# Performance work log

Hardware: AMD Instinct MI355X
Metric: run time of the kernel (lower is better)

## Reference

```python
import jax, jax.numpy as jnp
import numpy as np

N_HEAD = 16
HEAD_SIZE = 64
N_EMBD = 1024
B, T = 4, 2048
THETA = 10000.0


def _rope_cos_sin(t_len, dim):
    # freqs: (dim//2,), angles: (T, dim//2)
    inv = 1.0 / (THETA ** (jnp.arange(0, dim, 2, dtype=jnp.float32) / dim))
    ang = jnp.arange(t_len, dtype=jnp.float32)[:, None] * inv[None, :]
    return jnp.cos(ang), jnp.sin(ang)


def _apply_rope(x, cos, sin):
    # x: (B, H, T, hs) -> complex-pair rotation over last dim
    xr = x.reshape(*x.shape[:-1], -1, 2)
    x0, x1 = xr[..., 0], xr[..., 1]
    c = cos[None, None, :, :]
    s = sin[None, None, :, :]
    o0 = x0 * c - x1 * s
    o1 = x0 * s + x1 * c
    return jnp.stack([o0, o1], axis=-1).reshape(x.shape)


def setup_inputs() -> dict:
    key = jax.random.key(0)
    ks = jax.random.split(key, 5)
    scale = 1.0 / np.sqrt(N_EMBD)
    return {
        "x": jax.random.normal(ks[0], (B, T, N_EMBD), dtype=jnp.float32),
        "Wq": jax.random.normal(ks[1], (N_EMBD, N_HEAD * HEAD_SIZE), dtype=jnp.float32) * scale,
        "Wk": jax.random.normal(ks[2], (N_EMBD, N_HEAD * HEAD_SIZE), dtype=jnp.float32) * scale,
        "Wv": jax.random.normal(ks[3], (N_EMBD, N_HEAD * HEAD_SIZE), dtype=jnp.float32) * scale,
        "Wp": jax.random.normal(ks[4], (N_HEAD * HEAD_SIZE, N_EMBD), dtype=jnp.float32) * scale,
        "bp": jnp.zeros((N_EMBD,), dtype=jnp.float32),
    }


def reference(x, Wq, Wk, Wv, Wp, bp):
    Bx, Tx, C = x.shape
    q = (x @ Wq).reshape(Bx, Tx, N_HEAD, HEAD_SIZE).transpose(0, 2, 1, 3)
    k = (x @ Wk).reshape(Bx, Tx, N_HEAD, HEAD_SIZE).transpose(0, 2, 1, 3)
    v = (x @ Wv).reshape(Bx, Tx, N_HEAD, HEAD_SIZE).transpose(0, 2, 1, 3)
    cos, sin = _rope_cos_sin(Tx, HEAD_SIZE)
    q = _apply_rope(q, cos, sin)
    k = _apply_rope(k, cos, sin)
    wei = jnp.einsum('bhqd,bhkd->bhqk', q, k) * (HEAD_SIZE ** -0.5)
    causal = jnp.tril(jnp.ones((Tx, Tx), dtype=bool))
    wei = jnp.where(causal[None, None, :, :], wei, -jnp.inf)
    wei = jax.nn.softmax(wei, axis=-1)
    out = jnp.einsum('bhqk,bhkd->bhqd', wei, v)
    out = out.transpose(0, 2, 1, 3).reshape(Bx, Tx, N_HEAD * HEAD_SIZE)
    return out @ Wp + bp
```

## Files before the change

### kernel.cpp

```cpp
#include <hip/hip_runtime.h>
#include <hip/hip_bf16.h>

#define NH 16
#define HS 64
#define CE 1024
#define BB 4
#define TT 2048

typedef __bf16 bf16;
typedef __bf16 v8bf __attribute__((ext_vector_type(8)));
typedef __bf16 v4bf __attribute__((ext_vector_type(4)));
typedef __bf16 v2bf __attribute__((ext_vector_type(2)));
typedef float v4f __attribute__((ext_vector_type(4)));
typedef float v16f __attribute__((ext_vector_type(16)));

#define GLD16(gp, lp)                                                              \
    __builtin_amdgcn_global_load_lds((const __attribute__((address_space(1))) void*)(gp), \
                                     (__attribute__((address_space(3))) void*)(lp), 16, 0, 0)

#define FENCE() __builtin_amdgcn_sched_barrier(0)
#define BARRIER() { FENCE(); __builtin_amdgcn_s_barrier(); FENCE(); }
#define VM4()  { asm volatile("s_waitcnt vmcnt(4)" ::: "memory"); FENCE(); }
#define VM8()  { asm volatile("s_waitcnt vmcnt(8)" ::: "memory"); FENCE(); }
#define VM0()  { asm volatile("s_waitcnt vmcnt(0)" ::: "memory"); FENCE(); }

__global__ __launch_bounds__(256) void prep_kernel(const float* __restrict__ x,
                                                   const float* __restrict__ W0,
                                                   const float* __restrict__ W1,
                                                   const float* __restrict__ W2,
                                                   const float* __restrict__ W3,
                                                   bf16* __restrict__ xb,
                                                   float2* __restrict__ csQ,
                                                   float2* __restrict__ csK,
                                                   bf16* __restrict__ dqkv,
                                                   bf16* __restrict__ dp) {
    __shared__ bf16 tile[64][66];
    const int bid = blockIdx.x;
    const int tid = threadIdx.x;
    if (bid < 4096) {
        int idx = (bid * 256 + tid) * 8;
        const float4* xp = (const float4*)(x + idx);
        float4 a = xp[0], b = xp[1];
        v8bf o;
        o[0] = (bf16)a.x; o[1] = (bf16)a.y; o[2] = (bf16)a.z; o[3] = (bf16)a.w;
        o[4] = (bf16)b.x; o[5] = (bf16)b.y; o[6] = (bf16)b.z; o[7] = (bf16)b.w;
        *(v8bf*)(xb + idx) = o;
    } else if (bid < 4352) {
        int idx = (bid - 4096) * 256 + tid;
        int t = idx >> 5, i = idx & 31;
        float inv = exp2f(-0.41524101186092034f * (float)i);
        float ang = (float)t * inv;
        float s, c;
        sincosf(ang, &s, &c);
        const float QS = 0.18033688011112042f;
        csK[idx] = make_float2(c, s);
        csQ[idx] = make_float2(c * QS, s * QS);
    } else {
        int idx = bid - 4352;
        int z = idx >> 8, rem = idx & 255;
        const float* W = (z == 0) ? W0 : (z == 1) ? W1 : (z == 2) ? W2 : W3;
        bf16* Wt = (z < 3) ? (dqkv + (size_t)z * 1024 * CE) : dp;
        int k0 = (rem & 15) * 64;
        int n0 = (rem >> 4) * 64;
        int tx = tid & 63;
        int ty = tid >> 6;
        for (int s = 0; s < 16; s++) {
            int r = s * 4 + ty;
            tile[r][tx] = (bf16)W[(size_t)(k0 + r) * CE + n0 + tx];
        }
        __syncthreads();
        for (int s = 0; s < 16; s++) {
            int r = s * 4 + ty;
            Wt[(size_t)(n0 + r) * CE + k0 + tx] = tile[tx][r];
        }
    }
}

#define GSTAGE(AD, BD, kk) {                                                        \
    _Pragma("unroll") for (int p = 0; p < 4; p++)                                   \
        GLD16(Ag + (kk) + (size_t)(p * 32) * CE, (AD) + p * 2048);                  \
    _Pragma("unroll") for (int p = 0; p < 4; p++)                                   \
        GLD16(Bg + (kk) + (size_t)(p * 32) * CE, (BD) + p * 2048); }

#define GCOMPUTE(ASrc, BSrc)                                                        \
    _Pragma("unroll")                                                               \
    for (int kh = 0; kh < 2; kh++) {                                                \
        v8bf af[4], bfr[4];                                                         \
        for (int i = 0; i < 4; i++) {                                               \
            int row = wr * 64 + i * 16 + lane15;                                    \
            af[i] = *(const v8bf*)(&ASrc[row * 64 + (((kh * 4 + quad) ^ (lane15 & 7)) * 8)]); \
        }                                                                           \
        for (int j = 0; j < 4; j++) {                                               \
            int row = wc * 64 + j * 16 + lane15;                                    \
            bfr[j] = *(const v8bf*)(&BSrc[row * 64 + (((kh * 4 + quad) ^ (lane15 & 7)) * 8)]); \
        }                                                                           \
        for (int i = 0; i < 4; i++)                                                 \
            for (int j = 0; j < 4; j++)                                             \
                acc[i][j] = __builtin_amdgcn_mfma_f32_16x16x32_bf16(af[i], bfr[j], acc[i][j], 0, 0, 0); \
    }

#define GEMM_PROLOG(Abuf, Bbuf)                                                     \
    __shared__ __align__(16) bf16 As0[128 * 64];                                    \
    __shared__ __align__(16) bf16 Bs0[128 * 64];                                    \
    __shared__ __align__(16) bf16 As1[128 * 64];                                    \
    __shared__ __align__(16) bf16 Bs1[128 * 64];                                    \
    const int tid = threadIdx.x;                                                    \
    const int lane = tid & 63, wave = tid >> 6;                                     \
    const int lane15 = lane & 15, quad = lane >> 4;                                 \
    const int wr = wave >> 1, wc = wave & 1;                                        \
    const int m0 = blockIdx.y * 128;                                                \
    const int n0 = blockIdx.x * 128;                                                \
    v4f acc[4][4] = {};                                                             \
    const int cm = tid >> 3;                                                        \
    const int ck = ((tid & 7) ^ (cm & 7)) * 8;                                      \
    const bf16* Ag = (Abuf) + (size_t)(m0 + cm) * CE + ck;                          \
    const bf16* Bg = (Bbuf) + (size_t)(n0 + cm) * CE + ck;                          \
    bf16* aD0 = &As0[wave * 512];                                                   \
    bf16* bD0 = &Bs0[wave * 512];                                                   \
    bf16* aD1 = &As1[wave * 512];                                                   \
    bf16* bD1 = &Bs1[wave * 512];

#define GEMM_KLOOP()                                                                \
    GSTAGE(aD0, bD0, 0);                                                            \
    for (int k0 = 0; k0 < CE; k0 += 128) {                                          \
        GSTAGE(aD1, bD1, k0 + 64);                                                  \
        VM8(); BARRIER();                                                           \
        GCOMPUTE(As0, Bs0);                                                         \
        BARRIER();                                                                  \
        GSTAGE(aD0, bD0, (k0 + 128) & 1023);                                        \
        VM8(); BARRIER();                                                           \
        GCOMPUTE(As1, Bs1);                                                         \
        BARRIER();                                                                  \
    }                                                                               \
    VM0();

__global__ __launch_bounds__(256) void gemm_qkv(const bf16* __restrict__ A,
                                                const bf16* __restrict__ Bt,
                                                bf16* __restrict__ Qb_, bf16* __restrict__ Kb_,
                                                bf16* __restrict__ Vt_,
                                                const float2* __restrict__ csQ,
                                                const float2* __restrict__ csK) {
    GEMM_PROLOG(A, Bt)
    GEMM_KLOOP()

    for (int i = 0; i < 4; i++) {
        for (int j = 0; j < 4; j++) {
            int gmb = m0 + wr * 64 + i * 16 + quad * 4;
            int gn = n0 + wc * 64 + j * 16 + lane15;
            int w = gn >> 10;
            int n = gn & 1023;
            int hh = n >> 6, d = n & 63;
            if (w < 2) {
                bf16* out = w ? Kb_ : Qb_;
                const float2* csRow = (w ? csK : csQ) + (d >> 1);
                const int par = gn & 1;
                const int dbase = d & ~1;
                const int b = gmb >> 11, tbase = gmb & 2047;
                const float xv0 = acc[i][j][0], xv1 = acc[i][j][1];
                const float xv2 = acc[i][j][2], xv3 = acc[i][j][3];
                const float pv0 = __shfl_xor(xv0, 1), pv1 = __shfl_xor(xv1, 1);
                const float pv2 = __shfl_xor(xv2, 1), pv3 = __shfl_xor(xv3, 1);
                const float xa = par ? xv2 : xv0, pa = par ? pv2 : pv0;
                const float xb2 = par ? xv3 : xv1, pb = par ? pv3 : pv1;
                const float ua = par ? pa : xa, va = par ? xa : pa;
                const float ub = par ? pb : xb2, vb = par ? xb2 : pb;
                const int ta = tbase + (par << 1), tb = ta + 1;
                const float2 csa = csRow[ta * 32];
                const float2 csb = csRow[tb * 32];
                v2bf sa, sb;
                sa[0] = (bf16)(ua * csa.x - va * csa.y);
                sa[1] = (bf16)(ua * csa.y + va * csa.x);
                sb[0] = (bf16)(ub * csb.x - vb * csb.y);
                sb[1] = (bf16)(ub * csb.y + vb * csb.x);
                bf16* rowp = out + ((size_t)(b * NH + hh)) * TT * HS + dbase;
                *(v2bf*)(rowp + (size_t)ta * HS) = sa;
                *(v2bf*)(rowp + (size_t)tb * HS) = sb;
            } else {
                int b = gmb >> 11, t = gmb & 2047;
                v4bf pack;
                for (int r = 0; r < 4; r++) pack[r] = (bf16)acc[i][j][r];
                *(v4bf*)(&Vt_[(((size_t)(b * NH + hh)) * HS + d) * TT + t]) = pack;
            }
        }
    }
}

__global__ __launch_bounds__(256) void gemm_proj(const bf16* __restrict__ A,
                                                 const bf16* __restrict__ Bt,
                                                 float* __restrict__ Pout,
                                                 const float* __restrict__ bias) {
    GEMM_PROLOG(A, Bt)

    float bb[4];
#pragma unroll
    for (int j = 0; j < 4; j++) bb[j] = bias[n0 + wc * 64 + j * 16 + lane15];

    GEMM_KLOOP()

    for (int i = 0; i < 4; i++) {
        for (int j = 0; j < 4; j++) {
            int gmb = m0 + wr * 64 + i * 16 + quad * 4;
            int gn = n0 + wc * 64 + j * 16 + lane15;
            for (int r = 0; r < 4; r++)
                Pout[(size_t)(gmb + r) * CE + gn] = acc[i][j][r] + bb[j];
        }
    }
}

#define ASTAGE(KD, VD, kv) {                                        \
    GLD16(kg + (size_t)(kv) * HS, (KD));                            \
    GLD16(kg + (size_t)((kv) + 32) * HS, (KD) + 2048);              \
    GLD16(vg + (kv), (VD));                                         \
    GLD16(vg + (kv) + 32 * TT, (VD) + 2048); }

#define ACOMPUTE(KS, VS, KVB)                                                       \
    _Pragma("unroll")                                                               \
    for (int sub = 0; sub < 2; sub++) {                                             \
        const int kvs = (KVB) + sub * 32;                                           \
        if (kvs > q0) break;                                                        \
        const bool diag = (kvs == q0);                                              \
        v16f s = {};                                                                \
        __builtin_amdgcn_s_setprio(1);                                              \
        for (int m = 0; m < 4; m++) {                                               \
            v8bf afr = *(const v8bf*)(&KS[(sub * 32 + lane31) * 64 +                \
                                          (((m << 1) | h) ^ (lane31 & 7)) * 8]);    \
            s = __builtin_amdgcn_mfma_f32_32x32x16_bf16(afr, qf[m], s, 0, 0, 0);    \
        }                                                                           \
        __builtin_amdgcn_s_setprio(0);                                              \
        float p[16];                                                                \
        if (diag) {                                                                 \
            for (int r = 0; r < 16; r++) {                                          \
                int kvr = (r & 3) + 8 * (r >> 2) + 4 * h;                           \
                p[r] = exp2f((kvr <= lane31) ? s[r] : -3.0e38f);                    \
            }                                                                       \
        } else {                                                                    \
            for (int r = 0; r < 16; r++) p[r] = exp2f(s[r]);                        \
        }                                                                           \
        float a8[8];                                                                \
        for (int r = 0; r < 8; r++) a8[r] = p[r] + p[r + 8];                        \
        l_i += ((a8[0] + a8[1]) + (a8[2] + a8[3])) + ((a8[4] + a8[5]) + (a8[6] + a8[7])); \
        union { v4bf v; unsigned long long u; } ch[4];                              \
        for (int g = 0; g < 4; g++)                                                 \
            for (int rr = 0; rr < 4; rr++)                                          \
                ch[g].v[rr] = (bf16)p[g * 4 + rr];                                  \
        __builtin_amdgcn_s_setprio(1);                                              \
        for (int t2 = 0; t2 < 2; t2++) {                                            \
            unsigned long long mine0 = ch[2 * t2].u, mine1 = ch[2 * t2 + 1].u;      \
            unsigned long long send = h ? mine0 : mine1;                            \
            unsigned long long recv = __shfl_xor(send, 32);                         \
            union { v8bf v; unsigned long long u[2]; } bfr2;                        \
            bfr2.u[0] = h ? recv : mine0;                                           \
            bfr2.u[1] = h ? mine1 : recv;                                           \
            int cidx = (((sub << 2) + (t2 << 1) + h) ^ (lane31 & 7)) * 8;           \
            v8bf va0 = *(const v8bf*)(&VS[lane31 * 64 + cidx]);                     \
            o0 = __builtin_amdgcn_mfma_f32_32x32x16_bf16(va0, bfr2.v, o0, 0, 0, 0); \
            v8bf va1 = *(const v8bf*)(&VS[(32 + lane31) * 64 + cidx]);              \
            o1 = __builtin_amdgcn_mfma_f32_32x32x16_bf16(va1, bfr2.v, o1, 0, 0, 0); \
        }                                                                           \
        __builtin_amdgcn_s_setprio(0);                                              \
    }

__global__ __launch_bounds__(256, 4) void attn_kernel(const bf16* __restrict__ Qb,
                                                      const bf16* __restrict__ Kb,
                                                      const bf16* __restrict__ Vt,
                                                      bf16* __restrict__ Ob) {
    __shared__ __align__(16) bf16 Ks0[64 * 64];
    __shared__ __align__(16) bf16 Vs0[64 * 64];
    __shared__ __align__(16) bf16 Ks1[64 * 64];
    __shared__ __align__(16) bf16 Vs1[64 * 64];
    const int tid = threadIdx.x, lane = tid & 63, wave = tid >> 6;
    const int lane31 = lane & 31, h = lane >> 5;
    const int bh = blockIdx.x & 63;
    const int qb = 15 - (int)(blockIdx.x >> 6);
    const int q0 = qb * 128 + wave * 32;
    const bf16* Qp = Qb + (size_t)bh * TT * HS;
    const bf16* Kp = Kb + (size_t)bh * TT * HS;
    const bf16* Vp = Vt + (size_t)bh * HS * TT;

    v8bf qf[4];
    for (int m = 0; m < 4; m++)
        qf[m] = *(const v8bf*)(Qp + (size_t)(q0 + lane31) * HS + m * 16 + h * 8);

    v16f o0 = {}, o1 = {};
    float l_i = 0.f;

    const int kr = tid >> 3, kc = tid & 7;
    const bf16* kg = Kp + kr * HS + ((kc ^ (kr & 7)) * 8);
    const bf16* vg = Vp + (size_t)kr * TT + ((kc ^ (kr & 7)) * 8);
    bf16* ksD0 = &Ks0[wave * 512];
    bf16* vsD0 = &Vs0[wave * 512];
    bf16* ksD1 = &Ks1[wave * 512];
    bf16* vsD1 = &Vs1[wave * 512];

    const int kv_max = qb * 128 + 96;
    ASTAGE(ksD0, vsD0, 0);
    for (int kv0 = 0; kv0 <= kv_max; kv0 += 128) {
        ASTAGE(ksD1, vsD1, kv0 + 64);
        VM4(); BARRIER();
        ACOMPUTE(Ks0, Vs0, kv0);
        BARRIER();
        ASTAGE(ksD0, vsD0, (kv0 + 128) & 2047);
        VM4(); BARRIER();
        ACOMPUTE(Ks1, Vs1, kv0 + 64);
        BARRIER();
    }
    VM0();

    const int b = bh >> 4, hh = bh & 15;
    const int q = q0 + lane31;
    float lt = l_i + __shfl_xor(l_i, 32);
    float invl = 1.f / lt;
    bf16* outRow = Ob + ((size_t)(b * TT + q)) * CE + hh * HS;
    for (int g = 0; g < 4; g++) {
        v4bf w0, w1;
        for (int rr = 0; rr < 4; rr++) {
            w0[rr] = (bf16)(o0[g * 4 + rr] * invl);
            w1[rr] = (bf16)(o1[g * 4 + rr] * invl);
        }
        *(v4bf*)(outRow + g * 8 + h * 4) = w0;
        *(v4bf*)(outRow + 32 + g * 8 + h * 4) = w1;
    }
}

extern "C" void kernel_launch(void* const* d_in, const int* in_sizes, int n_in,
                              void* d_out, int out_size, void* d_ws, size_t ws_size,
                              hipStream_t stream) {
    const float* x  = (const float*)d_in[0];
    const float* Wq = (const float*)d_in[1];
    const float* Wk = (const float*)d_in[2];
    const float* Wv = (const float*)d_in[3];
    const float* Wp = (const float*)d_in[4];
    const float* bp = (const float*)d_in[5];
    char* ws = (char*)d_ws;
    const size_t MB = 1024 * 1024;
    bf16* Xb    = (bf16*)(ws);
    bf16* WqkvT = (bf16*)(ws + 16 * MB);
    bf16* WpT   = (bf16*)(ws + 22 * MB);
    bf16* Qb    = (bf16*)(ws + 24 * MB);
    bf16* Kb    = (bf16*)(ws + 40 * MB);
    bf16* Vt    = (bf16*)(ws + 56 * MB);
    bf16* Ob    = (bf16*)(ws + 72 * MB);
    float2* csQ = (float2*)(ws + 72 * MB);
    float2* csK = (float2*)(ws + 72 * MB + 512 * 1024);

    prep_kernel<<<dim3(5376), dim3(256), 0, stream>>>(x, Wq, Wk, Wv, Wp, Xb, csQ, csK,
                                                      WqkvT, WpT);

    gemm_qkv<<<dim3(24, 64), dim3(256), 0, stream>>>(Xb, WqkvT, Qb, Kb, Vt, csQ, csK);

    attn_kernel<<<dim3(1024), dim3(256), 0, stream>>>(Qb, Kb, Vt, Ob);

    gemm_proj<<<dim3(8, 64), dim3(256), 0, stream>>>(Ob, WpT, (float*)d_out, bp);
}
```

Measured before the change: 261.6 us.

## Double attention block to 8 waves and swizzle GEMM tile order

Each attention block now has 512 threads (8 waves) covering 256 queries, so every staged K/V tile in LDS is reused by twice as many waves and each thread issues half as many global-to-LDS loads. The attention grid interleaves heavy and light causal query blocks to balance work across the device. Separately, the GEMM tiles are remapped in chunks of eight with a serpentine column order to improve L2 locality. The trade-off is a larger block with more registers and barriers, and the longest diagonal blocks get longer.

```diff
diff --git a/kernel.cpp b/kernel.cpp
--- a/kernel.cpp
+++ b/kernel.cpp
@@ -20,7 +20,7 @@
 
 #define FENCE() __builtin_amdgcn_sched_barrier(0)
 #define BARRIER() { FENCE(); __builtin_amdgcn_s_barrier(); FENCE(); }
-#define VM4()  { asm volatile("s_waitcnt vmcnt(4)" ::: "memory"); FENCE(); }
+#define VM2()  { asm volatile("s_waitcnt vmcnt(2)" ::: "memory"); FENCE(); }
 #define VM8()  { asm volatile("s_waitcnt vmcnt(8)" ::: "memory"); FENCE(); }
 #define VM0()  { asm volatile("s_waitcnt vmcnt(0)" ::: "memory"); FENCE(); }
 
@@ -108,8 +108,14 @@
     const int lane = tid & 63, wave = tid >> 6;                                     \
     const int lane15 = lane & 15, quad = lane >> 4;                                 \
     const int wr = wave >> 1, wc = wave & 1;                                        \
-    const int m0 = blockIdx.y * 128;                                                \
-    const int n0 = blockIdx.x * 128;                                                \
+    const int fid = blockIdx.y * gridDim.x + blockIdx.x;                            \
+    const int bchunk = (gridDim.x * gridDim.y) >> 3;                                \
+    const int swzb = (fid & 7) * bchunk + (fid >> 3);                               \
+    const int bmy = swzb / gridDim.x;                                               \
+    const int bnx0 = swzb % gridDim.x;                                              \
+    const int bnx = (bmy & 1) ? (gridDim.x - 1 - bnx0) : bnx0;                      \
+    const int m0 = bmy * 128;                                                       \
+    const int n0 = bnx * 128;                                                       \
     v4f acc[4][4] = {};                                                             \
     const int cm = tid >> 3;                                                        \
     const int ck = ((tid & 7) ^ (cm & 7)) * 8;                                      \
@@ -209,9 +215,7 @@
 
 #define ASTAGE(KD, VD, kv) {                                        \
     GLD16(kg + (size_t)(kv) * HS, (KD));                            \
-    GLD16(kg + (size_t)((kv) + 32) * HS, (KD) + 2048);              \
-    GLD16(vg + (kv), (VD));                                         \
-    GLD16(vg + (kv) + 32 * TT, (VD) + 2048); }
+    GLD16(vg + (kv), (VD)); }
 
 #define ACOMPUTE(KS, VS, KVB)                                                       \
     _Pragma("unroll")                                                               \
@@ -260,7 +264,7 @@
         __builtin_amdgcn_s_setprio(0);                                              \
     }
 
-__global__ __launch_bounds__(256, 4) void attn_kernel(const bf16* __restrict__ Qb,
+__global__ __launch_bounds__(512, 4) void attn_kernel(const bf16* __restrict__ Qb,
                                                       const bf16* __restrict__ Kb,
                                                       const bf16* __restrict__ Vt,
                                                       bf16* __restrict__ Ob) {
@@ -270,9 +274,12 @@
     __shared__ __align__(16) bf16 Vs1[64 * 64];
     const int tid = threadIdx.x, lane = tid & 63, wave = tid >> 6;
     const int lane31 = lane & 31, h = lane >> 5;
-    const int bh = blockIdx.x & 63;
-    const int qb = 15 - (int)(blockIdx.x >> 6);
-    const int q0 = qb * 128 + wave * 32;
+    const int bid = blockIdx.x;
+    const int x8 = bid & 7, jj = bid >> 3;
+    const int bh = x8 + 8 * (jj >> 3);
+    const int s9 = jj & 7;
+    const int qb = (s9 & 1) ? (s9 >> 1) : (7 - (s9 >> 1));
+    const int q0 = qb * 256 + wave * 32;
     const bf16* Qp = Qb + (size_t)bh * TT * HS;
     const bf16* Kp = Kb + (size_t)bh * TT * HS;
     const bf16* Vp = Vt + (size_t)bh * HS * TT;
@@ -292,15 +299,15 @@
     bf16* ksD1 = &Ks1[wave * 512];
     bf16* vsD1 = &Vs1[wave * 512];
 
-    const int kv_max = qb * 128 + 96;
+    const int kv_end = (qb + 1) * 256;
     ASTAGE(ksD0, vsD0, 0);
-    for (int kv0 = 0; kv0 <= kv_max; kv0 += 128) {
+    for (int kv0 = 0; kv0 < kv_end; kv0 += 128) {
         ASTAGE(ksD1, vsD1, kv0 + 64);
-        VM4(); BARRIER();
+        VM2(); BARRIER();
         ACOMPUTE(Ks0, Vs0, kv0);
         BARRIER();
         ASTAGE(ksD0, vsD0, (kv0 + 128) & 2047);
-        VM4(); BARRIER();
+        VM2(); BARRIER();
         ACOMPUTE(Ks1, Vs1, kv0 + 64);
         BARRIER();
     }
@@ -348,7 +355,7 @@
 
     gemm_qkv<<<dim3(24, 64), dim3(256), 0, stream>>>(Xb, WqkvT, Qb, Kb, Vt, csQ, csK);
 
-    attn_kernel<<<dim3(1024), dim3(256), 0, stream>>>(Qb, Kb, Vt, Ob);
+    attn_kernel<<<dim3(512), dim3(512), 0, stream>>>(Qb, Kb, Vt, Ob);
 
     gemm_proj<<<dim3(8, 64), dim3(256), 0, stream>>>(Ob, WpT, (float*)d_out, bp);
 }
```

After: 283.7 us. 1.08x slower.
